# Performance work log

Hardware: AMD Instinct MI355X
Metric: run time of the kernel (lower is better)

The kernel has to match this reference:

```python
import jax, jax.numpy as jnp
import numpy as np

N_EMBD = 768
N_HEAD = 12
LN_EPS = 1e-5

def _gelu_tanh(x):
    # 0.5*x*(1+tanh(sqrt(2/pi)*(x+0.044715*x^3)))
    c = 0.7978845608028654
    return 0.5 * x * (1.0 + jnp.tanh(c * (x + 0.044715 * x * x * x)))

def _layernorm(x, g, b):
    mu = jnp.mean(x, axis=-1, keepdims=True)
    var = jnp.mean(jnp.square(x - mu), axis=-1, keepdims=True)
    return (x - mu) * jax.lax.rsqrt(var + LN_EPS) * g + b

def setup_inputs() -> dict:
    key = jax.random.key(0)
    ks = jax.random.split(key, 8)
    C = N_EMBD
    s = 0.02
    return {
        "x": jax.random.normal(ks[0], (4, 2048, C), jnp.float32),
        "ln1_g": jnp.ones((C,), jnp.float32),
        "ln1_b": jnp.zeros((C,), jnp.float32),
        "attn_w": jax.random.normal(ks[1], (3 * C, C), jnp.float32) * s,
        "attn_b": jnp.zeros((3 * C,), jnp.float32),
        "proj_w": jax.random.normal(ks[2], (C, C), jnp.float32) * s,
        "proj_b": jnp.zeros((C,), jnp.float32),
        "ln2_g": jnp.ones((C,), jnp.float32),
        "ln2_b": jnp.zeros((C,), jnp.float32),
        "fc_w": jax.random.normal(ks[3], (4 * C, C), jnp.float32) * s,
        "fc_b": jnp.zeros((4 * C,), jnp.float32),
        "fc2_w": jax.random.normal(ks[4], (C, 4 * C), jnp.float32) * s,
        "fc2_b": jnp.zeros((C,), jnp.float32),
    }

def reference(x, ln1_g, ln1_b, attn_w, attn_b, proj_w, proj_b,
              ln2_g, ln2_b, fc_w, fc_b, fc2_w, fc2_b):
    B, T, C = x.shape
    H = N_HEAD
    D = C // H

    # --- attention branch ---
    h = _layernorm(x, ln1_g, ln1_b)
    qkv = h @ attn_w.T + attn_b            # [B,T,3C]
    q, k, v = jnp.split(qkv, 3, axis=-1)
    q = q.reshape(B, T, H, D).transpose(0, 2, 1, 3)  # [B,H,T,D]
    k = k.reshape(B, T, H, D).transpose(0, 2, 1, 3)
    v = v.reshape(B, T, H, D).transpose(0, 2, 1, 3)

    att = jnp.einsum('bhqd,bhkd->bhqk', q, k) * (1.0 / np.sqrt(D))
    causal = jnp.tril(jnp.ones((T, T), bool))
    att = jnp.where(causal, att, -jnp.inf)
    att = jax.nn.softmax(att, axis=-1)
    y = jnp.einsum('bhqk,bhkd->bhqd', att, v)        # [B,H,T,D]
    y = y.transpose(0, 2, 1, 3).reshape(B, T, C)
    y = y @ proj_w.T + proj_b
    x = x + y

    # --- MLP branch ---
    h2 = _layernorm(x, ln2_g, ln2_b)
    m = _gelu_tanh(h2 @ fc_w.T + fc_b)
    m = m @ fc2_w.T + fc2_b
    return x + m
```

## Files before the change

### kernel.cpp

```cpp
#include <hip/hip_runtime.h>
#include <hip/hip_bf16.h>

#define N_EMBD 768
#define N_HEADS 12
#define HEAD_DIM 64

typedef __attribute__((ext_vector_type(4))) float f32x4;
typedef __attribute__((ext_vector_type(8))) short s16x8;

__device__ __forceinline__ float bf2f(unsigned short u) {
  union { unsigned int i; float f; } z;
  z.i = ((unsigned int)u) << 16;
  return z.f;
}

__device__ __forceinline__ void gload_lds16(const void* g, void* l) {
  __builtin_amdgcn_global_load_lds(
      (const __attribute__((address_space(1))) void*)g,
      (__attribute__((address_space(3))) void*)l, 16, 0, 0);
}

__device__ __forceinline__ float gelu_f(float x) {
  const float c = 0.7978845608028654f;
  float u = c * (x + 0.044715f * x * x * x);
  float t = 1.0f - 2.0f / (__expf(2.0f * u) + 1.0f);
  return 0.5f * x * (1.0f + t);
}

__global__ void cvt4_kernel(const float* __restrict__ s0, __hip_bfloat16* d0,
                            const float* __restrict__ s1, __hip_bfloat16* d1,
                            const float* __restrict__ s2, __hip_bfloat16* d2,
                            const float* __restrict__ s3, __hip_bfloat16* d3,
                            int n0, int n1, int n2, int n3) {
  int i = blockIdx.x * 256 + threadIdx.x;
  if (i < n0) { d0[i] = __float2bfloat16(s0[i]); return; }
  i -= n0;
  if (i < n1) { d1[i] = __float2bfloat16(s1[i]); return; }
  i -= n1;
  if (i < n2) { d2[i] = __float2bfloat16(s2[i]); return; }
  i -= n2;
  if (i < n3) d3[i] = __float2bfloat16(s3[i]);
}

__global__ __launch_bounds__(256) void ln_kernel(
    const float* __restrict__ x, const float* __restrict__ g,
    const float* __restrict__ b, __hip_bfloat16* __restrict__ out) {
  __shared__ float red[8];
  const int row = blockIdx.x;
  const int tid = threadIdx.x;
  const float* xr = x + (size_t)row * N_EMBD;
  float v0 = xr[tid], v1 = xr[tid + 256], v2 = xr[tid + 512];
  float s = v0 + v1 + v2;
#pragma unroll
  for (int m = 32; m >= 1; m >>= 1) s += __shfl_xor(s, m);
  if ((tid & 63) == 0) red[tid >> 6] = s;
  __syncthreads();
  float mu = (red[0] + red[1] + red[2] + red[3]) * (1.0f / 768.0f);
  float d0 = v0 - mu, d1 = v1 - mu, d2 = v2 - mu;
  float ss = d0 * d0 + d1 * d1 + d2 * d2;
  __syncthreads();
#pragma unroll
  for (int m = 32; m >= 1; m >>= 1) ss += __shfl_xor(ss, m);
  if ((tid & 63) == 0) red[4 + (tid >> 6)] = ss;
  __syncthreads();
  float var = (red[4] + red[5] + red[6] + red[7]) * (1.0f / 768.0f);
  float rstd = rsqrtf(var + 1e-5f);
  __hip_bfloat16* orow = out + (size_t)row * N_EMBD;
  orow[tid]       = __float2bfloat16(d0 * rstd * g[tid]       + b[tid]);
  orow[tid + 256] = __float2bfloat16(d1 * rstd * g[tid + 256] + b[tid + 256]);
  orow[tid + 512] = __float2bfloat16(d2 * rstd * g[tid + 512] + b[tid + 512]);
}

#define TILE_M 128
#define TILE_N 128
#define TILE_K 32

template <int EPI>
__global__ __launch_bounds__(256) void gemm_bt(
    const __hip_bfloat16* __restrict__ A, const __hip_bfloat16* __restrict__ W,
    const float* __restrict__ bias, const float* __restrict__ resid,
    __hip_bfloat16* __restrict__ outb, float* __restrict__ outf,
    int M, int N, int K) {
  __shared__ __hip_bfloat16 smA[2][TILE_M * TILE_K];
  __shared__ __hip_bfloat16 smB[2][TILE_N * TILE_K];
  const int tid = threadIdx.x;
  const int lane = tid & 63;
  const int wave = tid >> 6;

  const int nbx = gridDim.x;
  const int nwg = nbx * gridDim.y;
  int bid = blockIdx.y * nbx + blockIdx.x;
  if ((nwg & 7) == 0) bid = (bid & 7) * (nwg >> 3) + (bid >> 3);
  const int m0 = (bid / nbx) * TILE_M;
  const int n0 = (bid % nbx) * TILE_N;
  const int wr = wave >> 1, wc = wave & 1;

  f32x4 acc[4][4];
#pragma unroll
  for (int i = 0; i < 4; ++i)
#pragma unroll
    for (int j = 0; j < 4; ++j) acc[i][j] = f32x4{0.f, 0.f, 0.f, 0.f};

  const int ar0 = tid >> 2;
  const int ac0 = (tid & 3) * 8;
  const __hip_bfloat16* Abase0 = A + (size_t)(m0 + ar0) * K + ac0;
  const __hip_bfloat16* Abase1 = A + (size_t)(m0 + 64 + ar0) * K + ac0;
  const __hip_bfloat16* Wbase0 = W + (size_t)(n0 + ar0) * K + ac0;
  const __hip_bfloat16* Wbase1 = W + (size_t)(n0 + 64 + ar0) * K + ac0;

  auto stage = [&](int buf, int k0) {
    gload_lds16(Abase0 + k0, &smA[buf][wave * 512]);
    gload_lds16(Abase1 + k0, &smA[buf][2048 + wave * 512]);
    gload_lds16(Wbase0 + k0, &smB[buf][wave * 512]);
    gload_lds16(Wbase1 + k0, &smB[buf][2048 + wave * 512]);
  };

  const int rA = lane & 15;
  const int ko = (lane >> 4) * 8;
  const int nk = K / TILE_K;

  stage(0, 0);

  int cur = 0;
  for (int t = 0; t < nk; ++t) {
    asm volatile("s_waitcnt vmcnt(0)" ::: "memory");
    asm volatile("s_barrier" ::: "memory");
    if (t + 1 < nk) stage(cur ^ 1, (t + 1) * TILE_K);

    s16x8 af[4], bfr[4];
#pragma unroll
    for (int mi = 0; mi < 4; ++mi)
      af[mi] = *(const s16x8*)&smA[cur][(wr * 64 + mi * 16 + rA) * TILE_K + ko];
#pragma unroll
    for (int ni = 0; ni < 4; ++ni)
      bfr[ni] = *(const s16x8*)&smB[cur][(wc * 64 + ni * 16 + rA) * TILE_K + ko];
    __builtin_amdgcn_s_setprio(1);
#pragma unroll
    for (int mi = 0; mi < 4; ++mi)
#pragma unroll
      for (int ni = 0; ni < 4; ++ni)
        acc[mi][ni] = __builtin_amdgcn_mfma_f32_16x16x32_bf16(
            af[mi], bfr[ni], acc[mi][ni], 0, 0, 0);
    __builtin_amdgcn_s_setprio(0);
    cur ^= 1;
  }

  const int crow = (lane >> 4) * 4;
  const int ccol = lane & 15;
#pragma unroll
  for (int mi = 0; mi < 4; ++mi) {
#pragma unroll
    for (int ni = 0; ni < 4; ++ni) {
      const int col = n0 + wc * 64 + ni * 16 + ccol;
      const float bv = bias[col];
#pragma unroll
      for (int j = 0; j < 4; ++j) {
        const int row = m0 + wr * 64 + mi * 16 + crow + j;
        float v = acc[mi][ni][j] + bv;
        const size_t o = (size_t)row * N + col;
        if (EPI == 0) {
          outb[o] = __float2bfloat16(v);
        } else if (EPI == 1) {
          outb[o] = __float2bfloat16(gelu_f(v));
        } else {
          outf[o] = resid[o] + v;
        }
      }
    }
  }
}

#define BM3 256
#define BN3 256
#define BK3 64

template <int EPI>
__global__ __launch_bounds__(512, 2) void gemm256b(
    const __hip_bfloat16* __restrict__ A, const __hip_bfloat16* __restrict__ W,
    const float* __restrict__ bias,
    __hip_bfloat16* __restrict__ outb, int M, int N, int K) {
  __shared__ __align__(16) char lds[2][65536];
  const int tid = threadIdx.x;
  const int lane = tid & 63;
  const int wave = tid >> 6;
  const int wr = wave >> 2;
  const int wc = wave & 3;

  const int nbx = gridDim.x;
  const int nwg = nbx * gridDim.y;
  int bid = blockIdx.y * nbx + blockIdx.x;
  if ((nwg & 7) == 0) bid = (bid & 7) * (nwg >> 3) + (bid >> 3);
  const int m0 = (bid / nbx) * BM3;
  const int n0 = (bid % nbx) * BN3;

  f32x4 acc[8][4];
#pragma unroll
  for (int m = 0; m < 8; ++m)
#pragma unroll
    for (int n = 0; n < 4; ++n) acc[m][n] = f32x4{0.f, 0.f, 0.f, 0.f};

  auto stageA = [&](int buf, int t, int c) {
    const int g = c * 512 + tid;
    const int row = g >> 3;
    const int col = ((g & 7) ^ (row & 7)) * 8;
    gload_lds16(A + (size_t)(m0 + row) * K + t * BK3 + col,
                lds[buf] + (c * 512 + wave * 64) * 16);
  };
  auto stageB = [&](int buf, int t, int c) {
    const int g = c * 512 + tid;
    const int row = g >> 3;
    const int col = ((g & 7) ^ (row & 7)) * 8;
    gload_lds16(W + (size_t)(n0 + row) * K + t * BK3 + col,
                lds[buf] + 32768 + (c * 512 + wave * 64) * 16);
  };

  const int fr = lane & 15;
  const int fq = lane >> 4;
  const int nk = K / BK3;

#pragma unroll
  for (int c = 0; c < 4; ++c) { stageA(0, 0, c); stageB(0, 0, c); }

  int cur = 0;
  for (int t = 0; t < nk; ++t) {
    asm volatile("s_waitcnt vmcnt(0)" ::: "memory");
    asm volatile("s_barrier" ::: "memory");
    const char* Ab = lds[cur];
    const char* Bb = lds[cur] + 32768;
    const bool pre = (t + 1 < nk);

    if (pre) { stageA(cur ^ 1, t + 1, 0); stageB(cur ^ 1, t + 1, 0); }

    s16x8 bfr[4][2];
#pragma unroll
    for (int n = 0; n < 4; ++n)
#pragma unroll
      for (int kh = 0; kh < 2; ++kh) {
        const int row = wc * 64 + n * 16 + fr;
        const int gc = (kh * 4 + fq) ^ (row & 7);
        bfr[n][kh] = *(const s16x8*)(Bb + row * 128 + gc * 16);
      }

#pragma unroll
    for (int p = 0; p < 4; ++p) {
      if (pre && p > 0) { stageA(cur ^ 1, t + 1, p); stageB(cur ^ 1, t + 1, p); }
      s16x8 af[2][2];
#pragma unroll
      for (int i = 0; i < 2; ++i)
#pragma unroll
        for (int kh = 0; kh < 2; ++kh) {
          const int row = wr * 128 + (2 * p + i) * 16 + fr;
          const int gc = (kh * 4 + fq) ^ (row & 7);
          af[i][kh] = *(const s16x8*)(Ab + row * 128 + gc * 16);
        }
      __builtin_amdgcn_s_setprio(1);
#pragma unroll
      for (int i = 0; i < 2; ++i)
#pragma unroll
        for (int n = 0; n < 4; ++n)
#pragma unroll
          for (int kh = 0; kh < 2; ++kh)
            acc[2 * p + i][n] = __builtin_amdgcn_mfma_f32_16x16x32_bf16(
                af[i][kh], bfr[n][kh], acc[2 * p + i][n], 0, 0, 0);
      __builtin_amdgcn_s_setprio(0);
    }
    cur ^= 1;
  }

  const int crow = fq * 4;
#pragma unroll
  for (int m = 0; m < 8; ++m) {
#pragma unroll
    for (int n = 0; n < 4; ++n) {
      const int col = n0 + wc * 64 + n * 16 + fr;
      const float bv = bias[col];
#pragma unroll
      for (int j = 0; j < 4; ++j) {
        const int row = m0 + wr * 128 + m * 16 + crow + j;
        float v = acc[m][n][j] + bv;
        const size_t o = (size_t)row * N + col;
        if (EPI == 0) outb[o] = __float2bfloat16(v);
        else outb[o] = __float2bfloat16(gelu_f(v));
      }
    }
  }
}

#define AP 72

__global__ __launch_bounds__(256) void attn_mfma(
    const __hip_bfloat16* __restrict__ qkv, __hip_bfloat16* __restrict__ y,
    int T) {
  __shared__ __hip_bfloat16 ks[64 * AP];
  __shared__ __hip_bfloat16 vt[64 * AP];
  __shared__ __hip_bfloat16 ps[4][16 * AP];
  const int tid = threadIdx.x;
  const int lane = tid & 63;
  const int wave = tid >> 6;
  const int b = blockIdx.y / N_HEADS, h = blockIdx.y % N_HEADS;
  const int nq = T / 64;
  const int qa0 = blockIdx.x * 64;
  const int qb0 = (nq - 1 - blockIdx.x) * 64;
  const size_t ldq = 3 * N_EMBD;
  const __hip_bfloat16* qb_ = qkv + (size_t)b * T * ldq + h * HEAD_DIM;
  const __hip_bfloat16* kb = qb_ + N_EMBD;
  const __hip_bfloat16* vb = qb_ + 2 * N_EMBD;

  const int fr = lane & 15;
  const int fo = (lane >> 4) * 8;
  const int crow = (lane >> 4) * 4;

  const float qs = 0.125f * 1.44269504f;
  auto loadq = [&](int qrow, int o) -> s16x8 {
    s16x8 v = *(const s16x8*)(qb_ + (size_t)qrow * ldq + o);
    s16x8 r;
#pragma unroll
    for (int i = 0; i < 8; ++i) {
      float f = bf2f((unsigned short)v[i]) * qs;
      __hip_bfloat16 hb = __float2bfloat16(f);
      r[i] = *reinterpret_cast<short*>(&hb);
    }
    return r;
  };
  s16x8 qfa0 = loadq(qa0 + wave * 16 + fr, fo);
  s16x8 qfa1 = loadq(qa0 + wave * 16 + fr, fo + 32);
  s16x8 qfb0 = loadq(qb0 + wave * 16 + fr, fo);
  s16x8 qfb1 = loadq(qb0 + wave * 16 + fr, fo + 32);

  f32x4 oa[4], ob[4];
  float ma[4], la[4], mb[4], lb_[4];
#pragma unroll
  for (int j = 0; j < 4; ++j) {
    oa[j] = f32x4{0.f, 0.f, 0.f, 0.f};
    ob[j] = f32x4{0.f, 0.f, 0.f, 0.f};
    ma[j] = -1e30f; la[j] = 0.f; mb[j] = -1e30f; lb_[j] = 0.f;
  }

  auto process = [&](const s16x8& q0f, const s16x8& q1f, f32x4 (&o)[4],
                     float (&m_)[4], float (&l_)[4], int tq0, bool diag,
                     int kt) {
    f32x4 sv[4];
#pragma unroll
    for (int sub = 0; sub < 4; ++sub) {
      s16x8 b0 = *(const s16x8*)&ks[(sub * 16 + fr) * AP + fo];
      s16x8 b1 = *(const s16x8*)&ks[(sub * 16 + fr) * AP + 32 + fo];
      f32x4 acc = f32x4{0.f, 0.f, 0.f, 0.f};
      acc = __builtin_amdgcn_mfma_f32_16x16x32_bf16(q0f, b0, acc, 0, 0, 0);
      acc = __builtin_amdgcn_mfma_f32_16x16x32_bf16(q1f, b1, acc, 0, 0, 0);
      sv[sub] = acc;
    }
    if (diag) {
      const int wq0 = tq0 + wave * 16;
#pragma unroll
      for (int sub = 0; sub < 4; ++sub) {
        const int key = kt + sub * 16 + fr;
#pragma unroll
        for (int j = 0; j < 4; ++j)
          if (key > wq0 + crow + j) sv[sub][j] = -1e30f;
      }
    }
    float corr[4];
    bool anyresc = false;
#pragma unroll
    for (int j = 0; j < 4; ++j) {
      float t = fmaxf(fmaxf(sv[0][j], sv[1][j]), fmaxf(sv[2][j], sv[3][j]));
#pragma unroll
      for (int msk = 1; msk <= 8; msk <<= 1) t = fmaxf(t, __shfl_xor(t, msk));
      const bool resc = t > m_[j] + 8.0f;
      corr[j] = resc ? exp2f(m_[j] - t) : 1.0f;
      if (resc) m_[j] = t;
      anyresc = anyresc || resc;
    }
    float rs[4] = {0.f, 0.f, 0.f, 0.f};
#pragma unroll
    for (int sub = 0; sub < 4; ++sub) {
#pragma unroll
      for (int j = 0; j < 4; ++j) {
        float p = exp2f(sv[sub][j] - m_[j]);
        rs[j] += p;
        ps[wave][(crow + j) * AP + sub * 16 + fr] = __float2bfloat16(p);
      }
    }
#pragma unroll
    for (int j = 0; j < 4; ++j) {
#pragma unroll
      for (int msk = 1; msk <= 8; msk <<= 1) rs[j] += __shfl_xor(rs[j], msk);
      l_[j] = l_[j] * corr[j] + rs[j];
    }
    if (__any(anyresc)) {
#pragma unroll
      for (int ds = 0; ds < 4; ++ds)
#pragma unroll
        for (int j = 0; j < 4; ++j) o[ds][j] *= corr[j];
    }
    s16x8 pf0 = *(const s16x8*)&ps[wave][fr * AP + fo];
    s16x8 pf1 = *(const s16x8*)&ps[wave][fr * AP + 32 + fo];
#pragma unroll
    for (int ds = 0; ds < 4; ++ds) {
      s16x8 v0 = *(const s16x8*)&vt[(ds * 16 + fr) * AP + fo];
      s16x8 v1 = *(const s16x8*)&vt[(ds * 16 + fr) * AP + 32 + fo];
      o[ds] = __builtin_amdgcn_mfma_f32_16x16x32_bf16(pf0, v0, o[ds], 0, 0, 0);
      o[ds] = __builtin_amdgcn_mfma_f32_16x16x32_bf16(pf1, v1, o[ds], 0, 0, 0);
    }
  };

  for (int kt = 0; kt <= qb0; kt += 64) {
    __syncthreads();
#pragma unroll
    for (int j = 0; j < 2; ++j) {
      int c = j * 256 + tid;
      int key = c >> 3, d0 = (c & 7) * 8;
      s16x8 kv = *(const s16x8*)(kb + (size_t)(kt + key) * ldq + d0);
      *(s16x8*)&ks[key * AP + d0] = kv;
    }
#pragma unroll
    for (int j = 0; j < 2; ++j) {
      int d0 = (wave * 2 + j) * 8;
      s16x8 vv = *(const s16x8*)(vb + (size_t)(kt + lane) * ldq + d0);
#pragma unroll
      for (int i = 0; i < 8; ++i)
        vt[(d0 + i) * AP + lane] = ((const __hip_bfloat16*)&vv)[i];
    }
    __syncthreads();

    if (kt <= qa0) process(qfa0, qfa1, oa, ma, la, qa0, kt == qa0, kt);
    process(qfb0, qfb1, ob, mb, lb_, qb0, kt == qb0, kt);
  }

#pragma unroll
  for (int j = 0; j < 4; ++j) {
    const float inva = 1.0f / la[j];
    const float invb = 1.0f / lb_[j];
    __hip_bfloat16* ya =
        y + (size_t)(b * T + qa0 + wave * 16 + crow + j) * N_EMBD + h * HEAD_DIM;
    __hip_bfloat16* yb =
        y + (size_t)(b * T + qb0 + wave * 16 + crow + j) * N_EMBD + h * HEAD_DIM;
#pragma unroll
    for (int ds = 0; ds < 4; ++ds) {
      ya[ds * 16 + fr] = __float2bfloat16(oa[ds][j] * inva);
      yb[ds * 16 + fr] = __float2bfloat16(ob[ds][j] * invb);
    }
  }
}

extern "C" void kernel_launch(void* const* d_in, const int* in_sizes, int n_in,
                              void* d_out, int out_size, void* d_ws,
                              size_t ws_size, hipStream_t stream) {
  const int B = 4, T = 2048, C = N_EMBD;
  const int M = B * T;

  const float* x      = (const float*)d_in[0];
  const float* ln1_g  = (const float*)d_in[1];
  const float* ln1_b  = (const float*)d_in[2];
  const float* attn_w = (const float*)d_in[3];
  const float* attn_b = (const float*)d_in[4];
  const float* proj_w = (const float*)d_in[5];
  const float* proj_b = (const float*)d_in[6];
  const float* ln2_g  = (const float*)d_in[7];
  const float* ln2_b  = (const float*)d_in[8];
  const float* fc_w   = (const float*)d_in[9];
  const float* fc_b   = (const float*)d_in[10];
  const float* fc2_w  = (const float*)d_in[11];
  const float* fc2_b  = (const float*)d_in[12];
  float* out = (float*)d_out;

  char* p = (char*)d_ws;
  size_t off = 0;
  auto take = [&](size_t bytes) -> void* {
    void* q = p + off;
    off += (bytes + 1023) & ~(size_t)1023;
    return q;
  };

  __hip_bfloat16* wqkv  = (__hip_bfloat16*)take((size_t)3 * C * C * 2);
  __hip_bfloat16* wproj = (__hip_bfloat16*)take((size_t)C * C * 2);
  __hip_bfloat16* wfc   = (__hip_bfloat16*)take((size_t)4 * C * C * 2);
  __hip_bfloat16* wfc2  = (__hip_bfloat16*)take((size_t)4 * C * C * 2);
  __hip_bfloat16* hbuf  = (__hip_bfloat16*)take((size_t)M * C * 2);
  __hip_bfloat16* big   = (__hip_bfloat16*)take((size_t)M * 4 * C * 2);
  __hip_bfloat16* ybuf  = (__hip_bfloat16*)take((size_t)M * C * 2);
  float*          x1    = (float*)take((size_t)M * C * 4);

  {
    const int n0 = 3 * C * C, n1 = C * C, n2 = 4 * C * C, n3 = 4 * C * C;
    const int ntot = n0 + n1 + n2 + n3;
    cvt4_kernel<<<(ntot + 255) / 256, 256, 0, stream>>>(
        attn_w, wqkv, proj_w, wproj, fc_w, wfc, fc2_w, wfc2, n0, n1, n2, n3);
  }

  ln_kernel<<<M, 256, 0, stream>>>(x, ln1_g, ln1_b, hbuf);
  gemm256b<0><<<dim3(3 * C / BN3, M / BM3), 512, 0, stream>>>(
      hbuf, wqkv, attn_b, big, M, 3 * C, C);
  attn_mfma<<<dim3(T / 128, B * N_HEADS), 256, 0, stream>>>(big, ybuf, T);
  gemm_bt<2><<<dim3(C / TILE_N, M / TILE_M), 256, 0, stream>>>(
      ybuf, wproj, proj_b, x, nullptr, x1, M, C, C);
  ln_kernel<<<M, 256, 0, stream>>>(x1, ln2_g, ln2_b, hbuf);
  gemm256b<1><<<dim3(4 * C / BN3, M / BM3), 512, 0, stream>>>(
      hbuf, wfc, fc_b, big, M, 4 * C, C);
  gemm_bt<2><<<dim3(C / TILE_N, M / TILE_M), 256, 0, stream>>>(
      big, wfc2, fc2_b, x1, nullptr, out, M, C, 4 * C);
}
```

Measured before the change: 345.9 us.

## Transpose QK^T MFMA for per-lane softmax stats and prefetch next K/V tile

Swaps the MFMA operands so each lane holds one query column of the score tile. Each lane now keeps a single running max and sum, which cuts the cross-lane shuffle reductions from four per row group down to two. The next K/V tile is loaded into registers while the current tile is processed, to hide global-load latency behind compute. The V transpose into LDS now packs two keys into each 32-bit store. The cost is extra live registers for the prefetch buffers and shuffles to broadcast correction factors into the output layout.

Result: faster. 305.6 us (-11.6%).

```diff
diff --git a/kernel.cpp b/kernel.cpp
--- a/kernel.cpp
+++ b/kernel.cpp
@@ -328,70 +328,85 @@
   s16x8 qfb1 = loadq(qb0 + wave * 16 + fr, fo + 32);
 
   f32x4 oa[4], ob[4];
-  float ma[4], la[4], mb[4], lb_[4];
 #pragma unroll
   for (int j = 0; j < 4; ++j) {
     oa[j] = f32x4{0.f, 0.f, 0.f, 0.f};
     ob[j] = f32x4{0.f, 0.f, 0.f, 0.f};
-    ma[j] = -1e30f; la[j] = 0.f; mb[j] = -1e30f; lb_[j] = 0.f;
-  }
+  }
+  float m_a = -1e30f, l_a = 0.f, m_b = -1e30f, l_b = 0.f;
+
+  s16x8 kr0, kr1, vr0, vr1;
+  const int krow0 = tid >> 3;
+  const int kcol = (tid & 7) * 8;
+  const int vkey = 2 * (lane & 31);
+  const int vd0 = wave * 16 + (lane >> 5) * 8;
+
+  auto loadKV = [&](int kt) {
+    kr0 = *(const s16x8*)(kb + (size_t)(kt + krow0) * ldq + kcol);
+    kr1 = *(const s16x8*)(kb + (size_t)(kt + 32 + krow0) * ldq + kcol);
+    vr0 = *(const s16x8*)(vb + (size_t)(kt + vkey) * ldq + vd0);
+    vr1 = *(const s16x8*)(vb + (size_t)(kt + vkey + 1) * ldq + vd0);
+  };
+  auto writeKV = [&]() {
+    *(s16x8*)&ks[krow0 * AP + kcol] = kr0;
+    *(s16x8*)&ks[(32 + krow0) * AP + kcol] = kr1;
+#pragma unroll
+    for (int i = 0; i < 8; ++i) {
+      unsigned u = (unsigned short)vr0[i] | ((unsigned)(unsigned short)vr1[i] << 16);
+      *(unsigned*)&vt[(vd0 + i) * AP + vkey] = u;
+    }
+  };
 
   auto process = [&](const s16x8& q0f, const s16x8& q1f, f32x4 (&o)[4],
-                     float (&m_)[4], float (&l_)[4], int tq0, bool diag,
-                     int kt) {
+                     float& m_, float& l_, int tq0, bool diag, int kt) {
     f32x4 sv[4];
 #pragma unroll
     for (int sub = 0; sub < 4; ++sub) {
-      s16x8 b0 = *(const s16x8*)&ks[(sub * 16 + fr) * AP + fo];
-      s16x8 b1 = *(const s16x8*)&ks[(sub * 16 + fr) * AP + 32 + fo];
+      s16x8 k0 = *(const s16x8*)&ks[(sub * 16 + fr) * AP + fo];
+      s16x8 k1 = *(const s16x8*)&ks[(sub * 16 + fr) * AP + 32 + fo];
       f32x4 acc = f32x4{0.f, 0.f, 0.f, 0.f};
-      acc = __builtin_amdgcn_mfma_f32_16x16x32_bf16(q0f, b0, acc, 0, 0, 0);
-      acc = __builtin_amdgcn_mfma_f32_16x16x32_bf16(q1f, b1, acc, 0, 0, 0);
+      acc = __builtin_amdgcn_mfma_f32_16x16x32_bf16(k0, q0f, acc, 0, 0, 0);
+      acc = __builtin_amdgcn_mfma_f32_16x16x32_bf16(k1, q1f, acc, 0, 0, 0);
       sv[sub] = acc;
     }
+    const int qg = tq0 + wave * 16 + fr;
     if (diag) {
-      const int wq0 = tq0 + wave * 16;
-#pragma unroll
-      for (int sub = 0; sub < 4; ++sub) {
-        const int key = kt + sub * 16 + fr;
+#pragma unroll
+      for (int sub = 0; sub < 4; ++sub)
 #pragma unroll
         for (int j = 0; j < 4; ++j)
-          if (key > wq0 + crow + j) sv[sub][j] = -1e30f;
+          if (kt + sub * 16 + crow + j > qg) sv[sub][j] = -1e30f;
+    }
+    float t = fmaxf(fmaxf(sv[0][0], sv[0][1]), fmaxf(sv[0][2], sv[0][3]));
+#pragma unroll
+    for (int sub = 1; sub < 4; ++sub)
+      t = fmaxf(t, fmaxf(fmaxf(sv[sub][0], sv[sub][1]),
+                         fmaxf(sv[sub][2], sv[sub][3])));
+    t = fmaxf(t, __shfl_xor(t, 16));
+    t = fmaxf(t, __shfl_xor(t, 32));
+    const bool resc = t > m_ + 8.0f;
+    const float corr = resc ? exp2f(m_ - t) : 1.0f;
+    if (resc) m_ = t;
+    float rs = 0.f;
+#pragma unroll
+    for (int sub = 0; sub < 4; ++sub) {
+#pragma unroll
+      for (int j = 0; j < 4; ++j) {
+        float p = exp2f(sv[sub][j] - m_);
+        rs += p;
+        ps[wave][fr * AP + sub * 16 + crow + j] = __float2bfloat16(p);
       }
     }
-    float corr[4];
-    bool anyresc = false;
-#pragma unroll
-    for (int j = 0; j < 4; ++j) {
-      float t = fmaxf(fmaxf(sv[0][j], sv[1][j]), fmaxf(sv[2][j], sv[3][j]));
-#pragma unroll
-      for (int msk = 1; msk <= 8; msk <<= 1) t = fmaxf(t, __shfl_xor(t, msk));
-      const bool resc = t > m_[j] + 8.0f;
-      corr[j] = resc ? exp2f(m_[j] - t) : 1.0f;
-      if (resc) m_[j] = t;
-      anyresc = anyresc || resc;
-    }
-    float rs[4] = {0.f, 0.f, 0.f, 0.f};
-#pragma unroll
-    for (int sub = 0; sub < 4; ++sub) {
+    rs += __shfl_xor(rs, 16);
+    rs += __shfl_xor(rs, 32);
+    l_ = l_ * corr + rs;
+    if (__any(resc)) {
 #pragma unroll
       for (int j = 0; j < 4; ++j) {
-        float p = exp2f(sv[sub][j] - m_[j]);
-        rs[j] += p;
-        ps[wave][(crow + j) * AP + sub * 16 + fr] = __float2bfloat16(p);
+        const float cj = __shfl(corr, (lane & 0x30) | (crow + j));
+#pragma unroll
+        for (int ds = 0; ds < 4; ++ds) o[ds][j] *= cj;
       }
-    }
-#pragma unroll
-    for (int j = 0; j < 4; ++j) {
-#pragma unroll
-      for (int msk = 1; msk <= 8; msk <<= 1) rs[j] += __shfl_xor(rs[j], msk);
-      l_[j] = l_[j] * corr[j] + rs[j];
-    }
-    if (__any(anyresc)) {
-#pragma unroll
-      for (int ds = 0; ds < 4; ++ds)
-#pragma unroll
-        for (int j = 0; j < 4; ++j) o[ds][j] *= corr[j];
     }
     s16x8 pf0 = *(const s16x8*)&ps[wave][fr * AP + fo];
     s16x8 pf1 = *(const s16x8*)&ps[wave][fr * AP + 32 + fo];
@@ -404,33 +419,22 @@
     }
   };
 
+  loadKV(0);
   for (int kt = 0; kt <= qb0; kt += 64) {
     __syncthreads();
-#pragma unroll
-    for (int j = 0; j < 2; ++j) {
-      int c = j * 256 + tid;
-      int key = c >> 3, d0 = (c & 7) * 8;
-      s16x8 kv = *(const s16x8*)(kb + (size_t)(kt + key) * ldq + d0);
-      *(s16x8*)&ks[key * AP + d0] = kv;
-    }
-#pragma unroll
-    for (int j = 0; j < 2; ++j) {
-      int d0 = (wave * 2 + j) * 8;
-      s16x8 vv = *(const s16x8*)(vb + (size_t)(kt + lane) * ldq + d0);
-#pragma unroll
-      for (int i = 0; i < 8; ++i)
-        vt[(d0 + i) * AP + lane] = ((const __hip_bfloat16*)&vv)[i];
-    }
+    writeKV();
     __syncthreads();
-
-    if (kt <= qa0) process(qfa0, qfa1, oa, ma, la, qa0, kt == qa0, kt);
-    process(qfb0, qfb1, ob, mb, lb_, qb0, kt == qb0, kt);
+    if (kt + 64 <= qb0) loadKV(kt + 64);
+    if (kt <= qa0) process(qfa0, qfa1, oa, m_a, l_a, qa0, kt == qa0, kt);
+    process(qfb0, qfb1, ob, m_b, l_b, qb0, kt == qb0, kt);
   }
 
 #pragma unroll
   for (int j = 0; j < 4; ++j) {
-    const float inva = 1.0f / la[j];
-    const float invb = 1.0f / lb_[j];
+    const float la_j = __shfl(l_a, (lane & 0x30) | (crow + j));
+    const float lb_j = __shfl(l_b, (lane & 0x30) | (crow + j));
+    const float inva = 1.0f / la_j;
+    const float invb = 1.0f / lb_j;
     __hip_bfloat16* ya =
         y + (size_t)(b * T + qa0 + wave * 16 + crow + j) * N_EMBD + h * HEAD_DIM;
     __hip_bfloat16* yb =
```
